# Kernel optimization log

Hardware: AMD Instinct MI355X
Metric: run time of the kernel (lower is better)

The kernel has to match this reference:

```python
import jax, jax.numpy as jnp
import numpy as np

B, N, DIM, H = 1, 512, 384, 8
SK, SV, PK, PV = 16, 16, 4, 4
PAIR = 128
EPS = 1e-8


def _rand_rotations(key, b, n):
    m = jax.random.normal(key, (b, n, 3, 3), dtype=jnp.float32)
    q, _ = jnp.linalg.qr(m)  # orthonormal frames
    return q


def setup_inputs() -> dict:
    key = jax.random.key(0)
    ks = jax.random.split(key, 16)
    w = lambda k, shape: jax.random.normal(k, shape, dtype=jnp.float32) * 0.02
    inp = {
        "x": jax.random.normal(ks[0], (B, N, DIM), dtype=jnp.float32),
        "pairwise_repr": jax.random.normal(ks[1], (B, N, N, PAIR), dtype=jnp.float32),
        "rotations": _rand_rotations(ks[2], B, N),
        "translations": jax.random.normal(ks[3], (B, N, 3), dtype=jnp.float32),
        "W_sq": w(ks[4], (DIM, H * SK)),
        "W_sk": w(ks[5], (DIM, H * SK)),
        "W_sv": w(ks[6], (DIM, H * SV)),
        "W_pq": w(ks[7], (DIM, H * PK * 3)),
        "W_pk": w(ks[8], (DIM, H * PK * 3)),
        "W_pv": w(ks[9], (DIM, H * PV * 3)),
        "W_pair": w(ks[10], (PAIR, H)),
        "b_pair": jnp.zeros((H,), dtype=jnp.float32),
        # softplus(point_weights) == 1 at init, per the original log(e-1) init
        "point_weights": jnp.full((H,), float(np.log(np.e - 1.0)), dtype=jnp.float32),
        "W_out": w(ks[11], (H * (SV + PV * 3 + PV + PAIR), DIM)),
        "b_out": jnp.zeros((DIM,), dtype=jnp.float32),
    }
    return inp


def reference(x, pairwise_repr, rotations, translations,
              W_sq, W_sk, W_sv, W_pq, W_pk, W_pv,
              W_pair, b_pair, point_weights, W_out, b_out):
    b, n, _ = x.shape
    scalar_scale = (3 * SK) ** -0.5          # 3 logit terms
    point_scale = ((3 * PK) * (9.0 / 2.0)) ** -0.5
    pair_scale = 3.0 ** -0.5

    q_s = (x @ W_sq).reshape(b, n, H, SK)
    k_s = (x @ W_sk).reshape(b, n, H, SK)
    v_s = (x @ W_sv).reshape(b, n, H, SV)

    def to_global_points(W, d):
        p = (x @ W).reshape(b, n, H, d, 3)           # local-frame points
        p = jnp.einsum('bnhdc,bncr->bnhdr', p, rotations)
        return p + translations[:, :, None, None, :]  # global frame

    q_p = to_global_points(W_pq, PK)
    k_p = to_global_points(W_pk, PK)
    v_p = to_global_points(W_pv, PV)

    # scalar attention logits
    logits = jnp.einsum('bihd,bjhd->bhij', q_s, k_s) * scalar_scale
    # pairwise bias logits
    pair_bias = jnp.einsum('bijp,ph->bhij', pairwise_repr, W_pair) + b_pair[None, :, None, None]
    logits = logits + pair_bias * pair_scale
    # point-distance logits
    diff = q_p[:, :, None] - k_p[:, None]            # (b, i, j, h, d, 3)
    dist2 = jnp.sum(diff * diff, axis=(-1, -2))      # (b, i, j, h)
    pw = jax.nn.softplus(point_weights)              # (h,)
    logits = logits - 0.5 * point_scale * jnp.transpose(dist2, (0, 3, 1, 2)) * pw[None, :, None, None]

    attn = jax.nn.softmax(logits, axis=-1)           # (b, h, i, j)

    out_s = jnp.einsum('bhij,bjhd->bihd', attn, v_s).reshape(b, n, H * SV)
    out_pair = jnp.einsum('bhij,bijp->bihp', attn, pairwise_repr).reshape(b, n, H * PAIR)
    pts = jnp.einsum('bhij,bjhdc->bihdc', attn, v_p)  # global-frame value points
    # rotate back to local frame with R^T
    pts_local = jnp.einsum('bihdc,bicr->bihdr',
                           pts - translations[:, :, None, None, :],
                           jnp.swapaxes(rotations, -1, -2))
    pts_norm = jnp.sqrt(jnp.sum(pts_local ** 2, axis=-1) + EPS)

    feats = jnp.concatenate([
        out_s,
        pts_local.reshape(b, n, H * PV * 3),
        pts_norm.reshape(b, n, H * PV),
        out_pair,
    ], axis=-1)
    return feats @ W_out + b_out
```

## Files before the change

kernel.cpp:

```cpp
#include <hip/hip_runtime.h>
#include <hip/hip_bf16.h>
#include <math.h>

#define NN 512
#define DIMX 384
#define HH 8
#define PAIRD 128

#define SCALAR_SCALE 0.144337567297406f
#define POINT_SCALE  0.136082763487954f
#define PAIR_SCALE   0.577350269189626f

#define KSL 8
#define KPER 160
#define PCH 1264

__global__ __launch_bounds__(256) void k_bias(
    const float* __restrict__ pair, const float* __restrict__ Wpair,
    __hip_bfloat16* __restrict__ bias)
{
    const int jc = blockIdx.x & 3;
    const int i  = blockIdx.x >> 2;
    const int tid = threadIdx.x;
    const int b  = tid >> 5;
    const int pq = tid & 31;

    float wv[32];
    {
        const float4* W4 = (const float4*)(Wpair + pq * 32);
        #pragma unroll
        for (int q = 0; q < 8; ++q) {
            float4 w = W4[q];
            wv[q * 4 + 0] = w.x; wv[q * 4 + 1] = w.y;
            wv[q * 4 + 2] = w.z; wv[q * 4 + 3] = w.w;
        }
    }
    #pragma unroll
    for (int it = 0; it < 4; ++it) {
        const int j0 = jc * 128 + it * 32;
        float cur[32];
        #pragma unroll
        for (int r = 0; r < 4; ++r) {
            const int j = j0 + b + r * 8;
            float4 a = *(const float4*)&pair[((size_t)i * NN + j) * PAIRD + pq * 4];
            float ac[4] = {a.x, a.y, a.z, a.w};
            #pragma unroll
            for (int h = 0; h < 8; ++h) {
                float s = 0.f;
                #pragma unroll
                for (int p = 0; p < 4; ++p) s += ac[p] * wv[p * 8 + h];
                cur[r * 8 + h] = s;
            }
        }
        #pragma unroll
        for (int s5 = 0; s5 < 5; ++s5) {
            const int m = 16 >> s5;
            const bool up = (pq & m) != 0;
            #pragma unroll
            for (int u = 0; u < (16 >> s5); ++u) {
                float lo = cur[u], hi = cur[u + (16 >> s5)];
                float send = up ? lo : hi;
                float got  = __shfl_xor(send, m);
                cur[u] = up ? (hi + got) : (lo + got);
            }
        }
        const int j = j0 + b + (pq >> 3) * 8;
        bias[((size_t)i * NN + j) * 8 + (pq & 7)] = __float2bfloat16(cur[0]);
    }
}

__global__ __launch_bounds__(256) void k_proj_gemm(
    const float* __restrict__ x,
    const float* __restrict__ Wsq, const float* __restrict__ Wsk, const float* __restrict__ Wsv,
    const float* __restrict__ Wpq, const float* __restrict__ Wpk, const float* __restrict__ Wpv,
    float* __restrict__ qs, float* __restrict__ ks, float* __restrict__ vs,
    float* __restrict__ plq, float* __restrict__ plk, float* __restrict__ plv)
{
    const int m0 = blockIdx.x * 64;
    const int t  = blockIdx.y;
    int ldw, c0;
    const float* W;
    float* out;
    if (t < 12) {
        const float* Ws[3] = {Wsq, Wsk, Wsv};
        float* outs[3] = {qs, ks, vs};
        W = Ws[t >> 2]; out = outs[t >> 2]; c0 = (t & 3) * 32; ldw = 128;
    } else {
        const int u = t - 12;
        const float* Wp[3] = {Wpq, Wpk, Wpv};
        float* outp[3] = {plq, plk, plv};
        W = Wp[u / 3]; out = outp[u / 3]; c0 = (u % 3) * 32; ldw = 96;
    }
    const int tid = threadIdx.x;
    __shared__ float xs[32][68];
    __shared__ float Bs[32][36];
    const int tx = tid & 15, ty = tid >> 4;
    float acc[4][2] = {};

    for (int kt = 0; kt < DIMX; kt += 32) {
        #pragma unroll
        for (int it = 0; it < 2; ++it) {
            int l = tid + it * 256;
            int row = l >> 3, kq = l & 7;
            float4 a = *(const float4*)&x[(size_t)(m0 + row) * DIMX + kt + kq * 4];
            xs[kq*4+0][row] = a.x; xs[kq*4+1][row] = a.y;
            xs[kq*4+2][row] = a.z; xs[kq*4+3][row] = a.w;
        }
        {
            int kk = tid >> 3, nq = tid & 7;
            float4 b = *(const float4*)&W[(size_t)(kt + kk) * ldw + c0 + nq * 4];
            *(float4*)&Bs[kk][nq * 4] = b;
        }
        __syncthreads();
        #pragma unroll
        for (int k = 0; k < 32; ++k) {
            float4 a  = *(const float4*)&xs[k][ty * 4];
            float2 bv = *(const float2*)&Bs[k][tx * 2];
            acc[0][0] += a.x * bv.x; acc[0][1] += a.x * bv.y;
            acc[1][0] += a.y * bv.x; acc[1][1] += a.y * bv.y;
            acc[2][0] += a.z * bv.x; acc[2][1] += a.z * bv.y;
            acc[3][0] += a.w * bv.x; acc[3][1] += a.w * bv.y;
        }
        __syncthreads();
    }
    #pragma unroll
    for (int r = 0; r < 4; ++r) {
        float2 v = make_float2(acc[r][0], acc[r][1]);
        *(float2*)&out[(size_t)(m0 + ty * 4 + r) * ldw + c0 + tx * 2] = v;
    }
}

__global__ __launch_bounds__(256) void k_frames(
    const float* __restrict__ plq, const float* __restrict__ plk, const float* __restrict__ plv,
    const float* __restrict__ rot, const float* __restrict__ trans,
    float* __restrict__ qp, float* __restrict__ kp, float* __restrict__ vp)
{
    int g = blockIdx.x * 256 + threadIdx.x;
    int m = g >> 14;
    int rem = g & 16383;
    int i = rem >> 5;
    int p = rem & 31;
    const float* pl = (m == 0 ? plq : (m == 1 ? plk : plv));
    float*       o  = (m == 0 ? qp  : (m == 1 ? kp  : vp));
    const float* l = &pl[(size_t)i * 96 + p * 3];
    const float* R = &rot[(size_t)i * 9];
    const float* T = &trans[(size_t)i * 3];
    float l0 = l[0], l1 = l[1], l2 = l[2];
    float* op = o + (size_t)i * 96 + p * 3;
    #pragma unroll
    for (int c = 0; c < 3; ++c)
        op[c] = l0 * R[0 * 3 + c] + l1 * R[1 * 3 + c] + l2 * R[2 * 3 + c] + T[c];
}

__global__ __launch_bounds__(256) void k_attn(
    const float* __restrict__ pair,
    const float* __restrict__ qs, const float* __restrict__ ks,
    const float* __restrict__ qp, const float* __restrict__ kp,
    const float* __restrict__ vs, const float* __restrict__ vp,
    const __hip_bfloat16* __restrict__ bias,
    const float* __restrict__ bpair, const float* __restrict__ pwts,
    float* __restrict__ attnp)
{
    const int jc  = blockIdx.x;
    const int i   = blockIdx.y;
    const int tid = threadIdx.x;

    __shared__ float smem[5120];
    float* wtb  = smem;
    float* cbb  = smem + 576;
    float* qs_s = smem + 592;
    float* qp_s = smem + 720;

    if (tid < 32) ((float4*)qs_s)[tid] = ((const float4*)(qs + (size_t)i * 128))[tid];
    if (tid < 24) ((float4*)qp_s)[tid] = ((const float4*)(qp + (size_t)i * 96))[tid];
    __syncthreads();

    const int g   = tid & 7;
    const int jjL = tid >> 3;
    const int h2  = tid >> 5;
    const int jj2 = tid & 31;
    const int jg  = h2, pq = jj2;

    const float bp_h = bpair[g];
    const float pw_h = log1pf(__expf(pwts[g]));

    float m_run = -1e30f, l_run = 0.f;
    float4 accP[8];
    #pragma unroll
    for (int z = 0; z < 8; ++z) accP[z] = make_float4(0, 0, 0, 0);
    float4 accS = make_float4(0, 0, 0, 0);
    float4 accV = make_float4(0, 0, 0, 0);

    const float4* pair4 = (const float4*)pair;
    const float4* vs4   = (const float4*)vs;
    const float4* vp4   = (const float4*)vp;

    for (int t = 0; t < 4; ++t) {
        float* wt = wtb + (t & 1) * 288;
        float* cb = cbb + (t & 1) * 8;

        {
            const int j = jc * 128 + t * 32 + jjL;
            float bv = __bfloat162float(bias[((size_t)i * NN + j) * 8 + g]);
            float sc = 0.f;
            const float4* kr4 = (const float4*)(ks + (size_t)j * 128 + g * 16);
            const float4* qr4 = (const float4*)&qs_s[g * 16];
            #pragma unroll
            for (int q = 0; q < 4; ++q) {
                float4 kq = kr4[q], qq = qr4[q];
                sc += qq.x * kq.x + qq.y * kq.y + qq.z * kq.z + qq.w * kq.w;
            }
            float d2 = 0.f;
            const float4* kp4 = (const float4*)(kp + (size_t)j * 96 + g * 12);
            const float4* qp4 = (const float4*)&qp_s[g * 12];
            #pragma unroll
            for (int q = 0; q < 3; ++q) {
                float4 kq = kp4[q], qq = qp4[q];
                float dx = qq.x - kq.x, dy = qq.y - kq.y, dz = qq.z - kq.z, dw = qq.w - kq.w;
                d2 += dx * dx + dy * dy + dz * dz + dw * dw;
            }
            wt[g * 36 + jjL] = sc * SCALAR_SCALE + (bv + bp_h) * PAIR_SCALE
                             - 0.5f * POINT_SCALE * pw_h * d2;
        }
        __syncthreads();

        {
            float lg = wt[h2 * 36 + jj2];
            float tm = lg;
            #pragma unroll
            for (int off = 16; off > 0; off >>= 1) tm = fmaxf(tm, __shfl_xor(tm, off));
            float m_new = fmaxf(m_run, tm);
            float corr  = __expf(m_run - m_new);
            float p     = __expf(lg - m_new);
            float ps    = p;
            #pragma unroll
            for (int off = 16; off > 0; off >>= 1) ps += __shfl_xor(ps, off);
            l_run = l_run * corr + ps;
            m_run = m_new;
            wt[h2 * 36 + jj2] = p;
            if (jj2 == 0) cb[h2] = corr;
        }
        __syncthreads();

        #pragma unroll
        for (int z = 0; z < 8; ++z) {
            float c = cb[z];
            accP[z].x *= c; accP[z].y *= c; accP[z].z *= c; accP[z].w *= c;
        }
        {
            float c = cb[pq >> 2];
            accS.x *= c; accS.y *= c; accS.z *= c; accS.w *= c;
        }
        if (pq < 24) {
            float c = cb[pq / 3];
            accV.x *= c; accV.y *= c; accV.z *= c; accV.w *= c;
        }
        #pragma unroll
        for (int jo = 0; jo < 4; ++jo) {
            const int jl = jo * 8 + jg;
            const int jglob = jc * 128 + t * 32 + jl;
            float4 pr = pair4[((size_t)i * NN + jglob) * 32 + pq];
            #pragma unroll
            for (int z = 0; z < 8; ++z) {
                float a = wt[z * 36 + jl];
                accP[z].x += a * pr.x; accP[z].y += a * pr.y;
                accP[z].z += a * pr.z; accP[z].w += a * pr.w;
            }
            {
                float a = wt[(pq >> 2) * 36 + jl];
                float4 v = vs4[(size_t)jglob * 32 + pq];
                accS.x += a * v.x; accS.y += a * v.y; accS.z += a * v.z; accS.w += a * v.w;
            }
            if (pq < 24) {
                float a = wt[(pq / 3) * 36 + jl];
                float4 v = vp4[(size_t)jglob * 24 + pq];
                accV.x += a * v.x; accV.y += a * v.y; accV.z += a * v.z; accV.w += a * v.w;
            }
        }
    }
    __syncthreads();

    float* attnc = attnp + ((size_t)i * 4 + jc) * PCH;
    if (jj2 == 0) { attnc[1248 + h2] = m_run; attnc[1256 + h2] = l_run; }

    #pragma unroll
    for (int z = 0; z < 8; ++z) {
        accP[z].x += __shfl_xor(accP[z].x, 32); accP[z].y += __shfl_xor(accP[z].y, 32);
        accP[z].z += __shfl_xor(accP[z].z, 32); accP[z].w += __shfl_xor(accP[z].w, 32);
    }
    accS.x += __shfl_xor(accS.x, 32); accS.y += __shfl_xor(accS.y, 32);
    accS.z += __shfl_xor(accS.z, 32); accS.w += __shfl_xor(accS.w, 32);
    accV.x += __shfl_xor(accV.x, 32); accV.y += __shfl_xor(accV.y, 32);
    accV.z += __shfl_xor(accV.z, 32); accV.w += __shfl_xor(accV.w, 32);

    float4* redP = (float4*)smem;
    float4* redS = (float4*)(smem + 4224);
    float4* redV = (float4*)(smem + 4736);
    const int jgp = jg >> 1;
    if ((jg & 1) == 0) {
        #pragma unroll
        for (int z = 0; z < 8; ++z) redP[(jgp * 8 + z) * 32 + pq] = accP[z];
        redS[jgp * 32 + pq] = accS;
        if (pq < 24) redV[jgp * 24 + pq] = accV;
    }
    __syncthreads();

    {
        const int z = tid >> 5, p4 = tid & 31;
        float4 s = redP[z * 32 + p4];
        #pragma unroll
        for (int gg = 1; gg < 4; ++gg) {
            float4 v = redP[(gg * 8 + z) * 32 + p4];
            s.x += v.x; s.y += v.y; s.z += v.z; s.w += v.w;
        }
        *(float4*)&attnc[z * 128 + p4 * 4] = s;
    }
    if (tid < 32) {
        float4 s = redS[tid];
        #pragma unroll
        for (int gg = 1; gg < 4; ++gg) {
            float4 v = redS[gg * 32 + tid];
            s.x += v.x; s.y += v.y; s.z += v.z; s.w += v.w;
        }
        *(float4*)&attnc[1024 + tid * 4] = s;
    } else if (tid < 56) {
        const int pc = tid - 32;
        float4 s = redV[pc];
        #pragma unroll
        for (int gg = 1; gg < 4; ++gg) {
            float4 v = redV[gg * 24 + pc];
            s.x += v.x; s.y += v.y; s.z += v.z; s.w += v.w;
        }
        *(float4*)&attnc[1152 + pc * 4] = s;
    }
}

__global__ __launch_bounds__(256) void k_attn_merge(
    const float* __restrict__ attnp,
    const float* __restrict__ rot, const float* __restrict__ trans,
    float* __restrict__ feats)
{
    const int i = blockIdx.x;
    const int tid = threadIdx.x;
    __shared__ float sm_m[32], sm_l[32], sW[32], sL[8], pts_s[96];

    const float* base = attnp + (size_t)i * 4 * PCH;
    if (tid < 32) {
        int jcx = tid >> 3, h = tid & 7;
        sm_m[jcx * 8 + h] = base[jcx * PCH + 1248 + h];
        sm_l[jcx * 8 + h] = base[jcx * PCH + 1256 + h];
    }
    __syncthreads();
    if (tid < 8) {
        const int h = tid;
        float M = fmaxf(fmaxf(sm_m[h], sm_m[8 + h]), fmaxf(sm_m[16 + h], sm_m[24 + h]));
        float L = 0.f;
        #pragma unroll
        for (int jcx = 0; jcx < 4; ++jcx) {
            float w = __expf(sm_m[jcx * 8 + h] - M);
            L += sm_l[jcx * 8 + h] * w;
            sW[jcx * 8 + h] = w;
        }
        sL[h] = L;
    }
    __syncthreads();

    {
        const int h = tid >> 5, pq = tid & 31;
        float4 s = make_float4(0, 0, 0, 0);
        #pragma unroll
        for (int jcx = 0; jcx < 4; ++jcx) {
            float4 a = *(const float4*)&base[jcx * PCH + h * 128 + pq * 4];
            float w = sW[jcx * 8 + h];
            s.x += a.x * w; s.y += a.y * w; s.z += a.z * w; s.w += a.w * w;
        }
        float inv = 1.f / sL[h];
        s.x *= inv; s.y *= inv; s.z *= inv; s.w *= inv;
        ((float4*)&feats[(size_t)i * 1280 + 256])[tid] = s;
    }
    if (tid < 32) {
        const int h = tid >> 2;
        float4 s = make_float4(0, 0, 0, 0);
        #pragma unroll
        for (int jcx = 0; jcx < 4; ++jcx) {
            float4 a = *(const float4*)&base[jcx * PCH + 1024 + tid * 4];
            float w = sW[jcx * 8 + h];
            s.x += a.x * w; s.y += a.y * w; s.z += a.z * w; s.w += a.w * w;
        }
        float inv = 1.f / sL[h];
        s.x *= inv; s.y *= inv; s.z *= inv; s.w *= inv;
        ((float4*)&feats[(size_t)i * 1280])[tid] = s;
    } else if (tid < 56) {
        const int pc = tid - 32;
        const int h = pc / 3;
        float4 s = make_float4(0, 0, 0, 0);
        #pragma unroll
        for (int jcx = 0; jcx < 4; ++jcx) {
            float4 a = *(const float4*)&base[jcx * PCH + 1152 + pc * 4];
            float w = sW[jcx * 8 + h];
            s.x += a.x * w; s.y += a.y * w; s.z += a.z * w; s.w += a.w * w;
        }
        float inv = 1.f / sL[h];
        s.x *= inv; s.y *= inv; s.z *= inv; s.w *= inv;
        ((float4*)pts_s)[pc] = s;
    }
    __syncthreads();

    if (tid < 32) {
        const float* R = &rot[(size_t)i * 9];
        const float* T = &trans[(size_t)i * 3];
        float px = pts_s[tid * 3 + 0] - T[0];
        float py = pts_s[tid * 3 + 1] - T[1];
        float pz = pts_s[tid * 3 + 2] - T[2];
        float n2 = 0.f;
        float* fo = feats + (size_t)i * 1280;
        #pragma unroll
        for (int r = 0; r < 3; ++r) {
            float lr = px * R[r * 3 + 0] + py * R[r * 3 + 1] + pz * R[r * 3 + 2];
            fo[128 + tid * 3 + r] = lr;
            n2 += lr * lr;
        }
        fo[224 + tid] = sqrtf(n2 + 1e-8f);
    }
}

__global__ __launch_bounds__(256) void k_final_gemm(
    const float* __restrict__ feats, const float* __restrict__ Wout,
    float* __restrict__ partial)
{
    const int m0 = blockIdx.x * 128;
    const int n0 = blockIdx.y * 128;
    const int ks = blockIdx.z;
    const int tid = threadIdx.x;
    const int k0 = ks * KPER;
    __shared__ float As[16][132];
    __shared__ float Bs[16][132];
    const int tx = tid & 15, ty = tid >> 4;
    float acc[8][8] = {};

    for (int kt = 0; kt < KPER; kt += 16) {
        #pragma unroll
        for (int it = 0; it < 2; ++it) {
            const int l = tid + it * 256;
            const int row = l >> 2, kq = l & 3;
            float4 a = *(const float4*)&feats[(size_t)(m0 + row) * 1280 + k0 + kt + kq * 4];
            As[kq * 4 + 0][row] = a.x; As[kq * 4 + 1][row] = a.y;
            As[kq * 4 + 2][row] = a.z; As[kq * 4 + 3][row] = a.w;
            const int kk = l >> 5, nq = l & 31;
            float4 b = *(const float4*)&Wout[(size_t)(k0 + kt + kk) * 384 + n0 + nq * 4];
            *(float4*)&Bs[kk][nq * 4] = b;
        }
        __syncthreads();
        #pragma unroll
        for (int k = 0; k < 16; ++k) {
            float4 a0 = *(const float4*)&As[k][ty * 8];
            float4 a1 = *(const float4*)&As[k][ty * 8 + 4];
            float4 b0 = *(const float4*)&Bs[k][tx * 8];
            float4 b1 = *(const float4*)&Bs[k][tx * 8 + 4];
            float am[8] = {a0.x, a0.y, a0.z, a0.w, a1.x, a1.y, a1.z, a1.w};
            float bn[8] = {b0.x, b0.y, b0.z, b0.w, b1.x, b1.y, b1.z, b1.w};
            #pragma unroll
            for (int r = 0; r < 8; ++r)
                #pragma unroll
                for (int c = 0; c < 8; ++c)
                    acc[r][c] += am[r] * bn[c];
        }
        __syncthreads();
    }
    float* po = partial + (size_t)ks * (512 * 384);
    #pragma unroll
    for (int r = 0; r < 8; ++r) {
        *(float4*)&po[(size_t)(m0 + ty * 8 + r) * 384 + n0 + tx * 8]     = *(float4*)&acc[r][0];
        *(float4*)&po[(size_t)(m0 + ty * 8 + r) * 384 + n0 + tx * 8 + 4] = *(float4*)&acc[r][4];
    }
}

__global__ __launch_bounds__(256) void k_reduce(
    const float* __restrict__ partial, const float* __restrict__ bout,
    float* __restrict__ out)
{
    const int f = blockIdx.x * 256 + threadIdx.x;
    const int e = f * 4;
    const int col = e % 384;
    float4 acc = *(const float4*)&bout[col];
    #pragma unroll
    for (int s = 0; s < KSL; ++s) {
        float4 p = *(const float4*)&partial[(size_t)s * (512 * 384) + e];
        acc.x += p.x; acc.y += p.y; acc.z += p.z; acc.w += p.w;
    }
    *(float4*)&out[e] = acc;
}

extern "C" void kernel_launch(void* const* d_in, const int* in_sizes, int n_in,
                              void* d_out, int out_size, void* d_ws, size_t ws_size,
                              hipStream_t stream) {
    const float* x     = (const float*)d_in[0];
    const float* pair  = (const float*)d_in[1];
    const float* rot   = (const float*)d_in[2];
    const float* trans = (const float*)d_in[3];
    const float* Wsq   = (const float*)d_in[4];
    const float* Wsk   = (const float*)d_in[5];
    const float* Wsv   = (const float*)d_in[6];
    const float* Wpq   = (const float*)d_in[7];
    const float* Wpk   = (const float*)d_in[8];
    const float* Wpv   = (const float*)d_in[9];
    const float* Wpair = (const float*)d_in[10];
    const float* bpair = (const float*)d_in[11];
    const float* pwts  = (const float*)d_in[12];
    const float* Wout  = (const float*)d_in[13];
    const float* bout  = (const float*)d_in[14];

    float* ws    = (float*)d_ws;
    float* qs    = ws;
    float* ks    = qs + 512 * 128;
    float* vs    = ks + 512 * 128;
    float* qp    = vs + 512 * 128;
    float* kp    = qp + 512 * 96;
    float* vp    = kp + 512 * 96;
    float* feats = vp + 512 * 96;
    float* biasF = feats + 512 * 1280;
    float* attnp = biasF + 1048576;
    float* plq   = attnp + 2048 * PCH;
    float* plk   = plq + 512 * 96;
    float* plv   = plk + 512 * 96;
    __hip_bfloat16* bias = (__hip_bfloat16*)biasF;
    float* partial = biasF;

    k_bias<<<2048, 256, 0, stream>>>(pair, Wpair, bias);
    k_proj_gemm<<<dim3(8, 21), 256, 0, stream>>>(x, Wsq, Wsk, Wsv, Wpq, Wpk, Wpv,
                                                 qs, ks, vs, plq, plk, plv);
    k_frames<<<192, 256, 0, stream>>>(plq, plk, plv, rot, trans, qp, kp, vp);
    k_attn<<<dim3(4, 512), 256, 0, stream>>>(pair, qs, ks, qp, kp, vs, vp,
                                             bias, bpair, pwts, attnp);
    k_attn_merge<<<512, 256, 0, stream>>>(attnp, rot, trans, feats);
    k_final_gemm<<<dim3(4, 3, KSL), 256, 0, stream>>>(feats, Wout, partial);
    k_reduce<<<192, 256, 0, stream>>>(partial, bout, (float*)d_out);
}
```

Measured before the change: 134.2 us.

## Compute all 128 logits per chunk up front, dropping online-softmax rescaling

The attention kernel no longer walks the 128-key chunk in four 32-key steps with an online softmax. It now computes all 128 logits per head into shared memory first, then does a single max/exp/sum pass, then runs the accumulation loop over all 128 keys with no per-step correction factors. This cuts the barrier count from about eight to two and removes the accumulator rescaling multiplies. In exchange, the logit and pair loads are no longer interleaved, which may reduce latency hiding, and the shared-memory layout and reduction offsets change.

```diff
diff --git a/kernel.cpp b/kernel.cpp
--- a/kernel.cpp
+++ b/kernel.cpp
@@ -165,11 +165,10 @@
     const int i   = blockIdx.y;
     const int tid = threadIdx.x;
 
-    __shared__ float smem[5120];
-    float* wtb  = smem;
-    float* cbb  = smem + 576;
-    float* qs_s = smem + 592;
-    float* qp_s = smem + 720;
+    __shared__ float smem[4992];
+    float* lg   = smem;
+    float* qs_s = smem + 1056;
+    float* qp_s = smem + 1184;
 
     if (tid < 32) ((float4*)qs_s)[tid] = ((const float4*)(qs + (size_t)i * 128))[tid];
     if (tid < 24) ((float4*)qp_s)[tid] = ((const float4*)(qp + (size_t)i * 96))[tid];
@@ -181,30 +180,18 @@
     const int jj2 = tid & 31;
     const int jg  = h2, pq = jj2;
 
-    const float bp_h = bpair[g];
-    const float pw_h = log1pf(__expf(pwts[g]));
-
-    float m_run = -1e30f, l_run = 0.f;
-    float4 accP[8];
-    #pragma unroll
-    for (int z = 0; z < 8; ++z) accP[z] = make_float4(0, 0, 0, 0);
-    float4 accS = make_float4(0, 0, 0, 0);
-    float4 accV = make_float4(0, 0, 0, 0);
-
-    const float4* pair4 = (const float4*)pair;
-    const float4* vs4   = (const float4*)vs;
-    const float4* vp4   = (const float4*)vp;
-
-    for (int t = 0; t < 4; ++t) {
-        float* wt = wtb + (t & 1) * 288;
-        float* cb = cbb + (t & 1) * 8;
-
-        {
-            const int j = jc * 128 + t * 32 + jjL;
+    {
+        const float bp_h = bpair[g];
+        const float pw_h = log1pf(__expf(pwts[g]));
+        const float4* qr4 = (const float4*)&qs_s[g * 16];
+        const float4* qp4 = (const float4*)&qp_s[g * 12];
+        #pragma unroll
+        for (int t = 0; t < 4; ++t) {
+            const int jl = t * 32 + jjL;
+            const int j  = jc * 128 + jl;
             float bv = __bfloat162float(bias[((size_t)i * NN + j) * 8 + g]);
             float sc = 0.f;
             const float4* kr4 = (const float4*)(ks + (size_t)j * 128 + g * 16);
-            const float4* qr4 = (const float4*)&qs_s[g * 16];
             #pragma unroll
             for (int q = 0; q < 4; ++q) {
                 float4 kq = kr4[q], qq = qr4[q];
@@ -212,67 +199,62 @@
             }
             float d2 = 0.f;
             const float4* kp4 = (const float4*)(kp + (size_t)j * 96 + g * 12);
-            const float4* qp4 = (const float4*)&qp_s[g * 12];
             #pragma unroll
             for (int q = 0; q < 3; ++q) {
                 float4 kq = kp4[q], qq = qp4[q];
                 float dx = qq.x - kq.x, dy = qq.y - kq.y, dz = qq.z - kq.z, dw = qq.w - kq.w;
                 d2 += dx * dx + dy * dy + dz * dz + dw * dw;
             }
-            wt[g * 36 + jjL] = sc * SCALAR_SCALE + (bv + bp_h) * PAIR_SCALE
+            lg[g * 132 + jl] = sc * SCALAR_SCALE + (bv + bp_h) * PAIR_SCALE
                              - 0.5f * POINT_SCALE * pw_h * d2;
         }
-        __syncthreads();
-
-        {
-            float lg = wt[h2 * 36 + jj2];
-            float tm = lg;
-            #pragma unroll
-            for (int off = 16; off > 0; off >>= 1) tm = fmaxf(tm, __shfl_xor(tm, off));
-            float m_new = fmaxf(m_run, tm);
-            float corr  = __expf(m_run - m_new);
-            float p     = __expf(lg - m_new);
-            float ps    = p;
-            #pragma unroll
-            for (int off = 16; off > 0; off >>= 1) ps += __shfl_xor(ps, off);
-            l_run = l_run * corr + ps;
-            m_run = m_new;
-            wt[h2 * 36 + jj2] = p;
-            if (jj2 == 0) cb[h2] = corr;
-        }
-        __syncthreads();
-
-        #pragma unroll
-        for (int z = 0; z < 8; ++z) {
-            float c = cb[z];
-            accP[z].x *= c; accP[z].y *= c; accP[z].z *= c; accP[z].w *= c;
-        }
-        {
-            float c = cb[pq >> 2];
-            accS.x *= c; accS.y *= c; accS.z *= c; accS.w *= c;
-        }
-        if (pq < 24) {
-            float c = cb[pq / 3];
-            accV.x *= c; accV.y *= c; accV.z *= c; accV.w *= c;
-        }
-        #pragma unroll
-        for (int jo = 0; jo < 4; ++jo) {
+    }
+    __syncthreads();
+
+    float m_run, l_run;
+    {
+        float v0 = lg[h2 * 132 + jj2],      v1 = lg[h2 * 132 + 32 + jj2];
+        float v2 = lg[h2 * 132 + 64 + jj2], v3 = lg[h2 * 132 + 96 + jj2];
+        float m = fmaxf(fmaxf(v0, v1), fmaxf(v2, v3));
+        #pragma unroll
+        for (int off = 16; off > 0; off >>= 1) m = fmaxf(m, __shfl_xor(m, off));
+        float e0 = __expf(v0 - m), e1 = __expf(v1 - m);
+        float e2 = __expf(v2 - m), e3 = __expf(v3 - m);
+        float s = e0 + e1 + e2 + e3;
+        #pragma unroll
+        for (int off = 16; off > 0; off >>= 1) s += __shfl_xor(s, off);
+        m_run = m; l_run = s;
+        lg[h2 * 132 + jj2]      = e0; lg[h2 * 132 + 32 + jj2] = e1;
+        lg[h2 * 132 + 64 + jj2] = e2; lg[h2 * 132 + 96 + jj2] = e3;
+    }
+    __syncthreads();
+
+    float4 accP[8];
+    #pragma unroll
+    for (int z = 0; z < 8; ++z) accP[z] = make_float4(0, 0, 0, 0);
+    float4 accS = make_float4(0, 0, 0, 0);
+    float4 accV = make_float4(0, 0, 0, 0);
+    {
+        const float4* pair4 = (const float4*)pair;
+        const float4* vs4   = (const float4*)vs;
+        const float4* vp4   = (const float4*)vp;
+        for (int jo = 0; jo < 16; ++jo) {
             const int jl = jo * 8 + jg;
-            const int jglob = jc * 128 + t * 32 + jl;
+            const int jglob = jc * 128 + jl;
             float4 pr = pair4[((size_t)i * NN + jglob) * 32 + pq];
             #pragma unroll
             for (int z = 0; z < 8; ++z) {
-                float a = wt[z * 36 + jl];
+                float a = lg[z * 132 + jl];
                 accP[z].x += a * pr.x; accP[z].y += a * pr.y;
                 accP[z].z += a * pr.z; accP[z].w += a * pr.w;
             }
             {
-                float a = wt[(pq >> 2) * 36 + jl];
+                float a = lg[(pq >> 2) * 132 + jl];
                 float4 v = vs4[(size_t)jglob * 32 + pq];
                 accS.x += a * v.x; accS.y += a * v.y; accS.z += a * v.z; accS.w += a * v.w;
             }
             if (pq < 24) {
-                float a = wt[(pq / 3) * 36 + jl];
+                float a = lg[(pq / 3) * 132 + jl];
                 float4 v = vp4[(size_t)jglob * 24 + pq];
                 accV.x += a * v.x; accV.y += a * v.y; accV.z += a * v.z; accV.w += a * v.w;
             }
@@ -294,8 +276,8 @@
     accV.z += __shfl_xor(accV.z, 32); accV.w += __shfl_xor(accV.w, 32);
 
     float4* redP = (float4*)smem;
-    float4* redS = (float4*)(smem + 4224);
-    float4* redV = (float4*)(smem + 4736);
+    float4* redS = (float4*)(smem + 4096);
+    float4* redV = (float4*)(smem + 4608);
     const int jgp = jg >> 1;
     if ((jg & 1) == 0) {
         #pragma unroll
```

Result: slower. 163.0 us (+21.4%).
